# Optimization experiments

Hardware: AMD Instinct MI355X
Metric: run time of the kernel (lower is better)

## Reference

```python
import jax, jax.numpy as jnp
import numpy as np

H, E, K = 1024, 8, 2  # hidden_size, num_experts, top_k
B, S = 2, 4096


def setup_inputs() -> dict:
    key = jax.random.key(0)
    ks = jax.random.split(key, 5)
    s = 1.0 / np.sqrt(H)
    return {
        "x": jax.random.normal(ks[0], (B, S, H), dtype=jnp.float32),
        "ln_scale": jnp.ones((H,), jnp.float32),
        "ln_bias": jnp.zeros((H,), jnp.float32),
        "w1": (jax.random.normal(ks[1], (H, H), jnp.float32) * s),
        "b1": jnp.zeros((H,), jnp.float32),
        "w2": (jax.random.normal(ks[2], (H, E), jnp.float32) * s),
        "b2": jnp.zeros((E,), jnp.float32),
        "We": (jax.random.normal(ks[3], (E, H, H), jnp.float32) * s),
        "be": jnp.zeros((E, H), jnp.float32),
    }


def _layernorm(x, scale, bias, eps=1e-5):
    m = jnp.mean(x, axis=-1, keepdims=True)
    v = jnp.var(x, axis=-1, keepdims=True)
    return (x - m) * jax.lax.rsqrt(v + eps) * scale + bias


def reference(x, ln_scale, ln_bias, w1, b1, w2, b2, We, be):
    b, s, h = x.shape
    # --- router (BaseRouter): LN -> MLP -> softmax -> top-k -> renorm ---
    xn = _layernorm(x, ln_scale, ln_bias)
    hmid = jax.nn.relu(xn @ w1 + b1)
    logits = hmid @ w2 + b2                      # [B,S,E]
    probs = jax.nn.softmax(logits, axis=-1)
    topk_p, topk_i = jax.lax.top_k(probs, K)     # [B,S,K]
    topk_p = topk_p / jnp.sum(topk_p, axis=-1, keepdims=True)
    # sparse combine weights [B,S,E]: renormalized top-k gate, 0 elsewhere
    cw = jnp.sum(topk_p[..., None] * jax.nn.one_hot(topk_i, E, dtype=x.dtype), axis=-2)
    # --- expert dispatch / weighted combine ---
    t = b * s
    xf = x.reshape(t, h)
    cwf = cw.reshape(t, E)
    ye = jnp.einsum('th,ehd->etd', xf, We) + be[:, None, :]   # [E,T,H]
    out = jnp.einsum('te,etd->td', cwf, ye).reshape(b, s, h)
    # --- aux load-balance loss ---
    mean_p = jnp.mean(probs, axis=(0, 1))        # [E]
    aux = jnp.sum(mean_p * jnp.log(mean_p * E + 1e-9))
    return out, aux
```

## Files before the change

### kernel.cpp

```cpp
#include <hip/hip_runtime.h>
#include <hip/hip_fp16.h>

#define H 1024
#define E 8
#define TT 8192

typedef __attribute__((ext_vector_type(8))) short bf16x8;
typedef __attribute__((ext_vector_type(4))) float f32x4;

__device__ __forceinline__ unsigned short f2bf(float f) {
  unsigned int u = __float_as_uint(f);
  u += 0x7fffu + ((u >> 16) & 1u);
  return (unsigned short)(u >> 16);
}

__device__ __forceinline__ int swz(int row, int c) {
  return (row << 5) | (((c ^ (row >> 1)) & 3) << 3);
}

__device__ __forceinline__ void gld16(void* lds, const void* g) {
  __builtin_amdgcn_global_load_lds((const __attribute__((address_space(1))) void*)g,
                                   (__attribute__((address_space(3))) void*)lds, 16, 0, 0);
}

__global__ __launch_bounds__(256) void k_cast_we(const float* __restrict__ we, unsigned short* __restrict__ wet) {
  __shared__ unsigned short tile[32][33];
  int e = blockIdx.z;
  int kb = blockIdx.x << 5, nb = blockIdx.y << 5;
  int t = threadIdx.x;
  int cc = t & 31, rr = t >> 5;
  size_t base = (size_t)e * H * H;
#pragma unroll
  for (int r = 0; r < 4; ++r) {
    int k = kb + rr + (r << 3);
    tile[rr + (r << 3)][cc] = f2bf(we[base + (size_t)k * H + nb + cc]);
  }
  __syncthreads();
#pragma unroll
  for (int r = 0; r < 4; ++r) {
    int n = nb + rr + (r << 3);
    wet[base + (size_t)n * H + kb + cc] = tile[cc][rr + (r << 3)];
  }
}

__global__ __launch_bounds__(256) void k_cast_w1(const float* __restrict__ w1, const float* __restrict__ lsc,
                                                 const float* __restrict__ lbi, unsigned short* __restrict__ w1h,
                                                 unsigned short* __restrict__ w1l, float* __restrict__ part) {
  __shared__ float tile[32][33];
  __shared__ float red[8][33];
  int kb = blockIdx.x << 5, nb = blockIdx.y << 5;
  int t = threadIdx.x;
  int cc = t & 31, rr = t >> 5;
#pragma unroll
  for (int r = 0; r < 4; ++r) {
    int k = kb + rr + (r << 3);
    tile[rr + (r << 3)][cc] = w1[(size_t)k * H + nb + cc];
  }
  __syncthreads();
  float pp = 0.f;
#pragma unroll
  for (int r = 0; r < 4; ++r) {
    int kk = rr + (r << 3);
    pp = fmaf(lbi[kb + kk], tile[kk][cc], pp);
  }
  red[rr][cc] = pp;
  float scale = lsc[kb + cc];
  __syncthreads();
  if (rr == 0) {
    float s = 0.f;
#pragma unroll
    for (int j = 0; j < 8; ++j) s += red[j][cc];
    part[blockIdx.x * H + nb + cc] = s;
  }
#pragma unroll
  for (int r = 0; r < 4; ++r) {
    int n = nb + rr + (r << 3);
    float v = tile[cc][rr + (r << 3)] * scale;
    unsigned short h = f2bf(v);
    float hv = __uint_as_float((unsigned)h << 16);
    unsigned short l = f2bf(v - hv);
    w1h[(size_t)n * H + kb + cc] = h;
    w1l[(size_t)n * H + kb + cc] = l;
  }
}

__global__ __launch_bounds__(256) void k_b1b(const float* __restrict__ part, const float* __restrict__ b1,
                                             float* __restrict__ b1eff, int* __restrict__ cnt,
                                             double* __restrict__ psum) {
  int t = threadIdx.x;
  int n = (blockIdx.x << 8) + t;
  float s = b1[n];
  for (int j = 0; j < 32; ++j) s += part[j * H + n];
  b1eff[n] = s;
  if (blockIdx.x == 0 && t < E) { cnt[t] = 0; psum[t] = 0.0; }
}

__global__ __launch_bounds__(256) void k_stats(const float* __restrict__ x, float2* __restrict__ stats,
                                               unsigned short* __restrict__ xb) {
  int tok = blockIdx.x, t = threadIdx.x;
  const float4 v = *reinterpret_cast<const float4*>(&x[(size_t)tok * H + (t << 2)]);
  float s = v.x + v.y + v.z + v.w;
  float ss = v.x * v.x + v.y * v.y + v.z * v.z + v.w * v.w;
#pragma unroll
  for (int off = 32; off; off >>= 1) { s += __shfl_down(s, off); ss += __shfl_down(ss, off); }
  __shared__ float red[4][2];
  int lane = t & 63, wv = t >> 6;
  if (lane == 0) { red[wv][0] = s; red[wv][1] = ss; }
  __syncthreads();
  float fs = red[0][0] + red[1][0] + red[2][0] + red[3][0];
  float fss = red[0][1] + red[1][1] + red[2][1] + red[3][1];
  float mean = fs * (1.0f / H);
  float var = fss * (1.0f / H) - mean * mean;
  float rstd = rsqrtf(var + 1e-5f);
  if (t == 0) stats[tok] = make_float2(mean, rstd);
  ushort4 ob;
  ob.x = f2bf(v.x); ob.y = f2bf(v.y); ob.z = f2bf(v.z); ob.w = f2bf(v.w);
  *reinterpret_cast<ushort4*>(&xb[(size_t)tok * H + (t << 2)]) = ob;
}

__global__ __launch_bounds__(256) void k_router_mfma(
    const float* __restrict__ x, const float2* __restrict__ stats,
    const unsigned short* __restrict__ w1h, const unsigned short* __restrict__ w1l,
    const float* __restrict__ b1eff, const float* __restrict__ w2, float* __restrict__ plog) {
  __shared__ __align__(16) short Ah[4096], Al[4096], Bh[4096], Bl[4096];
  __shared__ float2 st[128];
  int t = threadIdx.x;
  int bm = blockIdx.x << 7, bn = blockIdx.y << 7;
  if (t < 128) st[t] = stats[bm + t];
  __syncthreads();
  int arow = t >> 1, ac0 = (t & 1) << 1;
  int brow = t >> 2, bc = t & 3;
  float2 mr = st[arow];
  float rs = mr.y, mb = -mr.x * mr.y;
  const float* xsrc = &x[(size_t)(bm + arow) * H + (ac0 << 3)];
  const unsigned short* s1 = &w1h[(size_t)(bn + brow) * H + (bc << 3)];
  const unsigned short* s2 = &w1h[(size_t)(bn + brow + 64) * H + (bc << 3)];
  const unsigned short* s3 = &w1l[(size_t)(bn + brow) * H + (bc << 3)];
  const unsigned short* s4 = &w1l[(size_t)(bn + brow + 64) * H + (bc << 3)];
  float4 va0 = *(const float4*)(xsrc + 0), va1 = *(const float4*)(xsrc + 4);
  float4 va2 = *(const float4*)(xsrc + 8), va3 = *(const float4*)(xsrc + 12);
  int4 vb0 = *(const int4*)s1, vb1 = *(const int4*)s2, vb2 = *(const int4*)s3, vb3 = *(const int4*)s4;
  int lane = t & 63, wv = t >> 6;
  int wr = (wv >> 1) << 6, wc = (wv & 1) << 6;
  int l15 = lane & 15, lgp = lane >> 4;
  f32x4 acc[4][4];
#pragma unroll
  for (int i = 0; i < 4; ++i)
#pragma unroll
    for (int j = 0; j < 4; ++j) acc[i][j] = f32x4{0.f, 0.f, 0.f, 0.f};
  for (int kt = 0; kt < 32; ++kt) {
    float zz[16];
    zz[0] = fmaf(va0.x, rs, mb); zz[1] = fmaf(va0.y, rs, mb);
    zz[2] = fmaf(va0.z, rs, mb); zz[3] = fmaf(va0.w, rs, mb);
    zz[4] = fmaf(va1.x, rs, mb); zz[5] = fmaf(va1.y, rs, mb);
    zz[6] = fmaf(va1.z, rs, mb); zz[7] = fmaf(va1.w, rs, mb);
    zz[8] = fmaf(va2.x, rs, mb); zz[9] = fmaf(va2.y, rs, mb);
    zz[10] = fmaf(va2.z, rs, mb); zz[11] = fmaf(va2.w, rs, mb);
    zz[12] = fmaf(va3.x, rs, mb); zz[13] = fmaf(va3.y, rs, mb);
    zz[14] = fmaf(va3.z, rs, mb); zz[15] = fmaf(va3.w, rs, mb);
    unsigned hw[8], lw[8];
#pragma unroll
    for (int p = 0; p < 8; ++p) {
      unsigned ua = __float_as_uint(zz[2 * p]), ub = __float_as_uint(zz[2 * p + 1]);
      hw[p] = (ua >> 16) | (ub & 0xffff0000u);
      float la = zz[2 * p] - __uint_as_float(ua & 0xffff0000u);
      float lb = zz[2 * p + 1] - __uint_as_float(ub & 0xffff0000u);
      lw[p] = (__float_as_uint(la) >> 16) | (__float_as_uint(lb) & 0xffff0000u);
    }
    __syncthreads();
    *(int4*)&Ah[swz(arow, ac0)] = make_int4(hw[0], hw[1], hw[2], hw[3]);
    *(int4*)&Ah[swz(arow, ac0 + 1)] = make_int4(hw[4], hw[5], hw[6], hw[7]);
    *(int4*)&Al[swz(arow, ac0)] = make_int4(lw[0], lw[1], lw[2], lw[3]);
    *(int4*)&Al[swz(arow, ac0 + 1)] = make_int4(lw[4], lw[5], lw[6], lw[7]);
    *(int4*)&Bh[swz(brow, bc)] = vb0;
    *(int4*)&Bh[swz(brow + 64, bc)] = vb1;
    *(int4*)&Bl[swz(brow, bc)] = vb2;
    *(int4*)&Bl[swz(brow + 64, bc)] = vb3;
    __syncthreads();
    if (kt + 1 < 32) {
      xsrc += 32; s1 += 32; s2 += 32; s3 += 32; s4 += 32;
      va0 = *(const float4*)(xsrc + 0); va1 = *(const float4*)(xsrc + 4);
      va2 = *(const float4*)(xsrc + 8); va3 = *(const float4*)(xsrc + 12);
      vb0 = *(const int4*)s1; vb1 = *(const int4*)s2; vb2 = *(const int4*)s3; vb3 = *(const int4*)s4;
    }
    bf16x8 bh[4], bl[4];
#pragma unroll
    for (int j = 0; j < 4; ++j) {
      bh[j] = *(const bf16x8*)&Bh[swz(wc + (j << 4) + l15, lgp)];
      bl[j] = *(const bf16x8*)&Bl[swz(wc + (j << 4) + l15, lgp)];
    }
#pragma unroll
    for (int i = 0; i < 4; ++i) {
      bf16x8 ah = *(const bf16x8*)&Ah[swz(wr + (i << 4) + l15, lgp)];
      bf16x8 al = *(const bf16x8*)&Al[swz(wr + (i << 4) + l15, lgp)];
#pragma unroll
      for (int j = 0; j < 4; ++j) {
        acc[i][j] = __builtin_amdgcn_mfma_f32_16x16x32_bf16(ah, bh[j], acc[i][j], 0, 0, 0);
        acc[i][j] = __builtin_amdgcn_mfma_f32_16x16x32_bf16(ah, bl[j], acc[i][j], 0, 0, 0);
        acc[i][j] = __builtin_amdgcn_mfma_f32_16x16x32_bf16(al, bh[j], acc[i][j], 0, 0, 0);
      }
    }
  }
  float w2r[4][8], b1r[4];
#pragma unroll
  for (int j = 0; j < 4; ++j) {
    int col = bn + wc + (j << 4) + l15;
    float4 p0 = *(const float4*)&w2[(size_t)col * E];
    float4 p1 = *(const float4*)&w2[(size_t)col * E + 4];
    w2r[j][0] = p0.x; w2r[j][1] = p0.y; w2r[j][2] = p0.z; w2r[j][3] = p0.w;
    w2r[j][4] = p1.x; w2r[j][5] = p1.y; w2r[j][6] = p1.z; w2r[j][7] = p1.w;
    b1r[j] = b1eff[col];
  }
#pragma unroll
  for (int i = 0; i < 4; ++i)
#pragma unroll
    for (int j = 0; j < 4; ++j)
#pragma unroll
      for (int r = 0; r < 4; ++r) acc[i][j][r] = fmaxf(acc[i][j][r] + b1r[j], 0.f);
  int wh = wc >> 6;
  size_t pbase = ((size_t)(blockIdx.y * 2 + wh) * TT + bm) * E;
#pragma unroll
  for (int e = 0; e < E; ++e) {
    float se[4][4];
#pragma unroll
    for (int i = 0; i < 4; ++i)
#pragma unroll
      for (int r = 0; r < 4; ++r)
        se[i][r] = acc[i][0][r] * w2r[0][e] + acc[i][1][r] * w2r[1][e] +
                   acc[i][2][r] * w2r[2][e] + acc[i][3][r] * w2r[3][e];
#pragma unroll
    for (int off = 1; off < 16; off <<= 1)
#pragma unroll
      for (int i = 0; i < 4; ++i)
#pragma unroll
        for (int r = 0; r < 4; ++r) se[i][r] += __shfl_xor(se[i][r], off);
    if (l15 == 0) {
#pragma unroll
      for (int i = 0; i < 4; ++i)
#pragma unroll
        for (int r = 0; r < 4; ++r) {
          int row = wr + (i << 4) + (lgp << 2) + r;
          plog[pbase + (size_t)row * E + e] = se[i][r];
        }
    }
  }
}

__global__ __launch_bounds__(256) void k_top(const float* __restrict__ plog, const float* __restrict__ b2,
                                             int* __restrict__ topE, float* __restrict__ topW,
                                             int* __restrict__ listIdx, float* __restrict__ listW,
                                             int* __restrict__ cnt, double* __restrict__ psum) {
  int t = threadIdx.x, lane = t & 63;
  int tok = (blockIdx.x << 8) + t;
  float lg[E], p[E];
  float4 ba = *reinterpret_cast<const float4*>(b2);
  float4 bb = *reinterpret_cast<const float4*>(b2 + 4);
  lg[0] = ba.x; lg[1] = ba.y; lg[2] = ba.z; lg[3] = ba.w;
  lg[4] = bb.x; lg[5] = bb.y; lg[6] = bb.z; lg[7] = bb.w;
#pragma unroll
  for (int nb = 0; nb < 16; ++nb) {
    const float* pp = &plog[((size_t)nb * TT + tok) * E];
    float4 q0 = *reinterpret_cast<const float4*>(pp);
    float4 q1 = *reinterpret_cast<const float4*>(pp + 4);
    lg[0] += q0.x; lg[1] += q0.y; lg[2] += q0.z; lg[3] += q0.w;
    lg[4] += q1.x; lg[5] += q1.y; lg[6] += q1.z; lg[7] += q1.w;
  }
  float m = lg[0];
#pragma unroll
  for (int e = 1; e < E; ++e) m = fmaxf(m, lg[e]);
  float s = 0.f;
#pragma unroll
  for (int e = 0; e < E; ++e) { p[e] = __expf(lg[e] - m); s += p[e]; }
  float inv = 1.f / s;
#pragma unroll
  for (int e = 0; e < E; ++e) p[e] *= inv;
  {
    float ps[E];
#pragma unroll
    for (int e = 0; e < E; ++e) ps[e] = p[e];
#pragma unroll
    for (int off = 1; off < 64; off <<= 1)
#pragma unroll
      for (int e = 0; e < E; ++e) ps[e] += __shfl_xor(ps[e], off);
    if (lane == 0)
#pragma unroll
      for (int e = 0; e < E; ++e) atomicAdd(&psum[e], (double)ps[e]);
  }
  int e0 = 0;
#pragma unroll
  for (int e = 1; e < E; ++e) if (p[e] > p[e0]) e0 = e;
  int e1 = (e0 == 0) ? 1 : 0;
#pragma unroll
  for (int e = 0; e < E; ++e) if (e != e0 && p[e] > p[e1]) e1 = e;
  float rsw = 1.f / (p[e0] + p[e1]);
  float w0 = p[e0] * rsw, w1v = p[e1] * rsw;
  topE[tok << 1] = e0; topE[(tok << 1) + 1] = e1;
  topW[tok << 1] = w0; topW[(tok << 1) + 1] = w1v;
  unsigned long long lt = (1ull << lane) - 1ull;
#pragma unroll
  for (int e = 0; e < E; ++e) {
    unsigned long long m0 = __ballot(e0 == e);
    unsigned long long m1 = __ballot(e1 == e);
    int n0 = __popcll(m0), total = n0 + __popcll(m1);
    if (total == 0) continue;
    int leader = __ffsll(m0 | m1) - 1;
    int base = 0;
    if (lane == leader) base = atomicAdd(&cnt[e], total);
    base = __shfl(base, leader);
    if (e0 == e) {
      int pos = e * TT + base + __popcll(m0 & lt);
      listIdx[pos] = (tok << 1); listW[pos] = w0;
    }
    if (e1 == e) {
      int pos = e * TT + base + n0 + __popcll(m1 & lt);
      listIdx[pos] = (tok << 1) | 1; listW[pos] = w1v;
    }
  }
}

#define WL_SLOTS 2560
__global__ __launch_bounds__(256) void k_sched(const int* __restrict__ cnt, int* __restrict__ workList) {
  int t = threadIdx.x;
  for (int i = t; i < WL_SLOTS; i += 256) workList[i] = -1;
  __syncthreads();
  if (t < E) {
    int e = t;
    int nb = (cnt[e] + 127) >> 7;
    int ov = 2048 + (e << 6);
    int g = 0;
    for (int bx = 0; bx < nb; ++bx) {
      for (int by = 0; by < 8; ++by) {
        int item = (e << 12) | (bx << 4) | by;
        int slot = (g < 256) ? ((g << 3) + e) : ov++;
        workList[slot] = item;
        ++g;
      }
    }
  }
}

__global__ __launch_bounds__(256) void k_expert_gemm(const unsigned short* __restrict__ xb,
                                                     const unsigned short* __restrict__ wet,
                                                     const int* __restrict__ listIdx, const float* __restrict__ listW,
                                                     const int* __restrict__ cnt, const int* __restrict__ workList,
                                                     unsigned short* __restrict__ ys) {
  int item = workList[blockIdx.x];
  if (item < 0) return;
  int e = item >> 12, bx = (item >> 4) & 255, by = item & 15;
  int c = cnt[e];
  int r0 = bx << 7, n0 = by << 7;
  __shared__ __align__(16) short A[2][4096], Bs[2][4096];
  __shared__ int gi[128];
  __shared__ float gw[128];
  int t = threadIdx.x;
  if (t < 128) {
    int rr = r0 + t;
    gi[t] = (rr < c) ? listIdx[e * TT + rr] : -1;
    gw[t] = (rr < c) ? listW[e * TT + rr] : 0.f;
  }
  __syncthreads();
  int w = t >> 6, lane = t & 63;
  int l15 = lane & 15, lgp = lane >> 4;
  int wr = (w >> 1) << 6, wc = (w & 1) << 6;
  int s0 = (w << 7) + lane, s1 = s0 + 64;
  int rA0 = s0 >> 2, cg0 = (s0 & 3) ^ ((rA0 >> 1) & 3);
  int rA1 = s1 >> 2, cg1 = (s1 & 3) ^ ((rA1 >> 1) & 3);
  int pk0 = gi[rA0], pk1 = gi[rA1];
  const unsigned short* srcA0 = xb + (size_t)((pk0 < 0) ? 0 : (pk0 >> 1)) * H + (cg0 << 3);
  const unsigned short* srcA1 = xb + (size_t)((pk1 < 0) ? 0 : (pk1 >> 1)) * H + (cg1 << 3);
  size_t wbase = (size_t)e * H * H;
  const unsigned short* srcB0 = wet + wbase + (size_t)(n0 + rA0) * H + (cg0 << 3);
  const unsigned short* srcB1 = wet + wbase + (size_t)(n0 + rA1) * H + (cg1 << 3);
  int d0 = (w << 10), d1 = d0 + 512;
  f32x4 acc[4][4];
#pragma unroll
  for (int i = 0; i < 4; ++i)
#pragma unroll
    for (int j = 0; j < 4; ++j) acc[i][j] = f32x4{0.f, 0.f, 0.f, 0.f};
  gld16(&A[0][d0], srcA0); gld16(&A[0][d1], srcA1);
  gld16(&Bs[0][d0], srcB0); gld16(&Bs[0][d1], srcB1);
#pragma unroll
  for (int kt = 0; kt < 32; ++kt) {
    const int cur = kt & 1, nxt = cur ^ 1;
    if (kt < 31) {
      const int ko = (kt + 1) << 5;
      gld16(&A[nxt][d0], srcA0 + ko); gld16(&A[nxt][d1], srcA1 + ko);
      gld16(&Bs[nxt][d0], srcB0 + ko); gld16(&Bs[nxt][d1], srcB1 + ko);
      asm volatile("s_waitcnt vmcnt(4)" ::: "memory");
    } else {
      asm volatile("s_waitcnt vmcnt(0)" ::: "memory");
    }
    __builtin_amdgcn_sched_barrier(0);
    __builtin_amdgcn_s_barrier();
    __builtin_amdgcn_sched_barrier(0);
    bf16x8 bq[4];
#pragma unroll
    for (int j = 0; j < 4; ++j) bq[j] = *(const bf16x8*)&Bs[cur][swz(wc + (j << 4) + l15, lgp)];
    bf16x8 aq[4];
#pragma unroll
    for (int i = 0; i < 4; ++i) aq[i] = *(const bf16x8*)&A[cur][swz(wr + (i << 4) + l15, lgp)];
    __builtin_amdgcn_s_setprio(1);
#pragma unroll
    for (int i = 0; i < 4; ++i)
#pragma unroll
      for (int j = 0; j < 4; ++j)
        acc[i][j] = __builtin_amdgcn_mfma_f32_16x16x32_bf16(aq[i], bq[j], acc[i][j], 0, 0, 0);
    __builtin_amdgcn_s_setprio(0);
    if (kt < 31) {
      __builtin_amdgcn_sched_barrier(0);
      __builtin_amdgcn_s_barrier();
    }
  }
#pragma unroll
  for (int i = 0; i < 4; ++i) {
#pragma unroll
    for (int r = 0; r < 4; ++r) {
      int row = wr + (i << 4) + (lgp << 2) + r;
      int pk = gi[row];
      if (pk < 0) continue;
      int tok = pk >> 1, slot = pk & 1;
      float wgt = gw[row];
      size_t ob = ((size_t)slot * TT + tok) * H + n0 + wc + l15;
#pragma unroll
      for (int j = 0; j < 4; ++j) ys[ob + (j << 4)] = __half_as_ushort(__float2half(wgt * acc[i][j][r]));
    }
  }
}

__global__ __launch_bounds__(256) void k_combine(const unsigned short* __restrict__ ys, const int* __restrict__ topE,
                                                 const float* __restrict__ topW, const float* __restrict__ be,
                                                 float* __restrict__ out) {
  int tok = blockIdx.x, t = threadIdx.x;
  int e0 = topE[tok << 1], e1 = topE[(tok << 1) + 1];
  float w0 = topW[tok << 1], w1v = topW[(tok << 1) + 1];
  int h = t << 2;
  size_t base = (size_t)tok * H + h;
  ushort4 a = *reinterpret_cast<const ushort4*>(&ys[base]);
  ushort4 b = *reinterpret_cast<const ushort4*>(&ys[(size_t)TT * H + base]);
  float4 b0 = *reinterpret_cast<const float4*>(&be[e0 * H + h]);
  float4 b1v = *reinterpret_cast<const float4*>(&be[e1 * H + h]);
  float4 o;
  o.x = __half2float(__ushort_as_half(a.x)) + __half2float(__ushort_as_half(b.x)) + w0 * b0.x + w1v * b1v.x;
  o.y = __half2float(__ushort_as_half(a.y)) + __half2float(__ushort_as_half(b.y)) + w0 * b0.y + w1v * b1v.y;
  o.z = __half2float(__ushort_as_half(a.z)) + __half2float(__ushort_as_half(b.z)) + w0 * b0.z + w1v * b1v.z;
  o.w = __half2float(__ushort_as_half(a.w)) + __half2float(__ushort_as_half(b.w)) + w0 * b0.w + w1v * b1v.w;
  *reinterpret_cast<float4*>(&out[base]) = o;
}

__global__ __launch_bounds__(64) void k_aux(const double* __restrict__ psum, float* __restrict__ outAux) {
  if (threadIdx.x == 0) {
    double a = 0.0;
    for (int e = 0; e < E; ++e) {
      double mp = psum[e] / (double)TT;
      a += mp * log(mp * (double)E + 1e-9);
    }
    outAux[0] = (float)a;
  }
}

extern "C" void kernel_launch(void* const* d_in, const int* in_sizes, int n_in, void* d_out, int out_size, void* d_ws,
                              size_t ws_size, hipStream_t stream) {
  const float* x = (const float*)d_in[0];
  const float* lsc = (const float*)d_in[1];
  const float* lbi = (const float*)d_in[2];
  const float* w1 = (const float*)d_in[3];
  const float* b1 = (const float*)d_in[4];
  const float* w2 = (const float*)d_in[5];
  const float* b2 = (const float*)d_in[6];
  const float* we = (const float*)d_in[7];
  const float* be = (const float*)d_in[8];
  float* out = (float*)d_out;
  char* ws = (char*)d_ws;

  char* p = ws;
  int* topE = (int*)p; p += TT * 2 * 4;
  float* topW = (float*)p; p += TT * 2 * 4;
  int* listIdx = (int*)p; p += E * TT * 4;
  float* listW = (float*)p; p += E * TT * 4;
  int* cnt = (int*)p; p += 256;
  double* psum = (double*)p; p += 2048;
  float* b1eff = (float*)p; p += H * 4;
  float* part = (float*)p; p += 32 * H * 4;
  int* workList = (int*)p; p += WL_SLOTS * 4;
  float2* stats = (float2*)p; p += TT * 8;
  unsigned short* xb = (unsigned short*)(ws + (2ull << 20));
  unsigned short* wet = (unsigned short*)(ws + (18ull << 20));
  unsigned short* w1h = (unsigned short*)(ws + (34ull << 20));
  unsigned short* w1l = (unsigned short*)(ws + (36ull << 20));
  float* plog = (float*)(ws + (38ull << 20));
  unsigned short* ys = (unsigned short*)(ws + (34ull << 20));

  k_cast_w1<<<dim3(32, 32), 256, 0, stream>>>(w1, lsc, lbi, w1h, w1l, part);
  k_b1b<<<4, 256, 0, stream>>>(part, b1, b1eff, cnt, psum);
  k_stats<<<TT, 256, 0, stream>>>(x, stats, xb);
  k_router_mfma<<<dim3(TT / 128, H / 128), 256, 0, stream>>>(x, stats, w1h, w1l, b1eff, w2, plog);
  k_top<<<TT / 256, 256, 0, stream>>>(plog, b2, topE, topW, listIdx, listW, cnt, psum);
  k_sched<<<1, 256, 0, stream>>>(cnt, workList);
  k_cast_we<<<dim3(32, 32, E), 256, 0, stream>>>(we, wet);
  k_expert_gemm<<<WL_SLOTS, 256, 0, stream>>>(xb, wet, listIdx, listW, cnt, workList, ys);
  k_combine<<<TT, 256, 0, stream>>>(ys, topE, topW, be, out);
  k_aux<<<1, 64, 0, stream>>>(psum, out + (size_t)TT * H);
}
```

Baseline: 220.0 us.

## Widen expert GEMM tile to 128x256 so each A tile feeds two B tiles

Each expert GEMM block now computes 256 output columns instead of 128, loading two B tiles per k-step while reusing the gathered A tile. The scheduler emits half as many work items per expert and the work-list is enlarged to fit the new overflow layout. This halves the redundant gathered-A global loads and the block count. In exchange it doubles the accumulator registers and LDS per block, which may lower occupancy, and leaves fewer blocks to spread across CUs.

Result: slower. 230.4 us (+4.7%).

```diff
diff --git a/kernel.cpp b/kernel.cpp
--- a/kernel.cpp
+++ b/kernel.cpp
@@ -318,7 +318,7 @@
   }
 }
 
-#define WL_SLOTS 2560
+#define WL_SLOTS 4096
 __global__ __launch_bounds__(256) void k_sched(const int* __restrict__ cnt, int* __restrict__ workList) {
   int t = threadIdx.x;
   for (int i = t; i < WL_SLOTS; i += 256) workList[i] = -1;
@@ -326,12 +326,11 @@
   if (t < E) {
     int e = t;
     int nb = (cnt[e] + 127) >> 7;
-    int ov = 2048 + (e << 6);
     int g = 0;
     for (int bx = 0; bx < nb; ++bx) {
-      for (int by = 0; by < 8; ++by) {
-        int item = (e << 12) | (bx << 4) | by;
-        int slot = (g < 256) ? ((g << 3) + e) : ov++;
+      for (int by2 = 0; by2 < 4; ++by2) {
+        int item = (e << 12) | (bx << 4) | by2;
+        int slot = (g < 256) ? ((g << 3) + e) : (2048 + (e << 8) + (g - 256));
         workList[slot] = item;
         ++g;
       }
@@ -346,10 +345,10 @@
                                                      unsigned short* __restrict__ ys) {
   int item = workList[blockIdx.x];
   if (item < 0) return;
-  int e = item >> 12, bx = (item >> 4) & 255, by = item & 15;
+  int e = item >> 12, bx = (item >> 4) & 255, by2 = item & 15;
   int c = cnt[e];
-  int r0 = bx << 7, n0 = by << 7;
-  __shared__ __align__(16) short A[2][4096], Bs[2][4096];
+  int r0 = bx << 7, n0 = by2 << 8;
+  __shared__ __align__(16) short A[2][4096], B0[2][4096], B1[2][4096];
   __shared__ int gi[128];
   __shared__ float gw[128];
   int t = threadIdx.x;
@@ -369,42 +368,54 @@
   const unsigned short* srcA0 = xb + (size_t)((pk0 < 0) ? 0 : (pk0 >> 1)) * H + (cg0 << 3);
   const unsigned short* srcA1 = xb + (size_t)((pk1 < 0) ? 0 : (pk1 >> 1)) * H + (cg1 << 3);
   size_t wbase = (size_t)e * H * H;
-  const unsigned short* srcB0 = wet + wbase + (size_t)(n0 + rA0) * H + (cg0 << 3);
-  const unsigned short* srcB1 = wet + wbase + (size_t)(n0 + rA1) * H + (cg1 << 3);
+  const unsigned short* srcB0a = wet + wbase + (size_t)(n0 + rA0) * H + (cg0 << 3);
+  const unsigned short* srcB0b = wet + wbase + (size_t)(n0 + rA1) * H + (cg1 << 3);
+  const unsigned short* srcB1a = wet + wbase + (size_t)(n0 + 128 + rA0) * H + (cg0 << 3);
+  const unsigned short* srcB1b = wet + wbase + (size_t)(n0 + 128 + rA1) * H + (cg1 << 3);
   int d0 = (w << 10), d1 = d0 + 512;
-  f32x4 acc[4][4];
+  f32x4 acc0[4][4], acc1[4][4];
 #pragma unroll
   for (int i = 0; i < 4; ++i)
 #pragma unroll
-    for (int j = 0; j < 4; ++j) acc[i][j] = f32x4{0.f, 0.f, 0.f, 0.f};
+    for (int j = 0; j < 4; ++j) { acc0[i][j] = f32x4{0.f, 0.f, 0.f, 0.f}; acc1[i][j] = f32x4{0.f, 0.f, 0.f, 0.f}; }
   gld16(&A[0][d0], srcA0); gld16(&A[0][d1], srcA1);
-  gld16(&Bs[0][d0], srcB0); gld16(&Bs[0][d1], srcB1);
+  gld16(&B0[0][d0], srcB0a); gld16(&B0[0][d1], srcB0b);
+  gld16(&B1[0][d0], srcB1a); gld16(&B1[0][d1], srcB1b);
 #pragma unroll
   for (int kt = 0; kt < 32; ++kt) {
     const int cur = kt & 1, nxt = cur ^ 1;
     if (kt < 31) {
       const int ko = (kt + 1) << 5;
       gld16(&A[nxt][d0], srcA0 + ko); gld16(&A[nxt][d1], srcA1 + ko);
-      gld16(&Bs[nxt][d0], srcB0 + ko); gld16(&Bs[nxt][d1], srcB1 + ko);
-      asm volatile("s_waitcnt vmcnt(4)" ::: "memory");
+      gld16(&B0[nxt][d0], srcB0a + ko); gld16(&B0[nxt][d1], srcB0b + ko);
+      gld16(&B1[nxt][d0], srcB1a + ko); gld16(&B1[nxt][d1], srcB1b + ko);
+      asm volatile("s_waitcnt vmcnt(6)" ::: "memory");
     } else {
       asm volatile("s_waitcnt vmcnt(0)" ::: "memory");
     }
     __builtin_amdgcn_sched_barrier(0);
     __builtin_amdgcn_s_barrier();
     __builtin_amdgcn_sched_barrier(0);
-    bf16x8 bq[4];
-#pragma unroll
-    for (int j = 0; j < 4; ++j) bq[j] = *(const bf16x8*)&Bs[cur][swz(wc + (j << 4) + l15, lgp)];
     bf16x8 aq[4];
 #pragma unroll
     for (int i = 0; i < 4; ++i) aq[i] = *(const bf16x8*)&A[cur][swz(wr + (i << 4) + l15, lgp)];
+    bf16x8 bq0[4], bq1[4];
+#pragma unroll
+    for (int j = 0; j < 4; ++j) {
+      bq0[j] = *(const bf16x8*)&B0[cur][swz(wc + (j << 4) + l15, lgp)];
+      bq1[j] = *(const bf16x8*)&B1[cur][swz(wc + (j << 4) + l15, lgp)];
+    }
     __builtin_amdgcn_s_setprio(1);
 #pragma unroll
     for (int i = 0; i < 4; ++i)
 #pragma unroll
       for (int j = 0; j < 4; ++j)
-        acc[i][j] = __builtin_amdgcn_mfma_f32_16x16x32_bf16(aq[i], bq[j], acc[i][j], 0, 0, 0);
+        acc0[i][j] = __builtin_amdgcn_mfma_f32_16x16x32_bf16(aq[i], bq0[j], acc0[i][j], 0, 0, 0);
+#pragma unroll
+    for (int i = 0; i < 4; ++i)
+#pragma unroll
+      for (int j = 0; j < 4; ++j)
+        acc1[i][j] = __builtin_amdgcn_mfma_f32_16x16x32_bf16(aq[i], bq1[j], acc1[i][j], 0, 0, 0);
     __builtin_amdgcn_s_setprio(0);
     if (kt < 31) {
       __builtin_amdgcn_sched_barrier(0);
@@ -422,7 +433,10 @@
       float wgt = gw[row];
       size_t ob = ((size_t)slot * TT + tok) * H + n0 + wc + l15;
 #pragma unroll
-      for (int j = 0; j < 4; ++j) ys[ob + (j << 4)] = __half_as_ushort(__float2half(wgt * acc[i][j][r]));
+      for (int j = 0; j < 4; ++j) {
+        ys[ob + (j << 4)] = __half_as_ushort(__float2half(wgt * acc0[i][j][r]));
+        ys[ob + 128 + (j << 4)] = __half_as_ushort(__float2half(wgt * acc1[i][j][r]));
+      }
     }
   }
 }
```
